# Kernel tuning notes

Measured on AMD Instinct MI355X. Metric: run time of the kernel, lower is better.

## Reference

```python
import jax, jax.numpy as jnp
import numpy as np

N = 100000
E = 1600000
IN_C, HID_C, OUT_C, NUM_CLASSES = 128, 64, 64, 40


def glorot(key, shape):
    lim = float(np.sqrt(6.0 / (shape[0] + shape[1])))
    return jax.random.uniform(key, shape, jnp.float32, -lim, lim)


def setup_inputs() -> dict:
    key = jax.random.key(0)
    ks = jax.random.split(key, 8)
    x = jax.random.normal(ks[0], (N, IN_C), jnp.float32)
    edge_index = jax.random.randint(ks[1], (2, E), 0, N, jnp.int64)
    return {
        "x": x,
        "edge_index": edge_index,
        "W1": glorot(ks[2], (IN_C, HID_C)),
        "b1": jnp.zeros((HID_C,), jnp.float32),
        "W2": glorot(ks[3], (HID_C, OUT_C)),
        "b2": jnp.zeros((OUT_C,), jnp.float32),
        "Wf": glorot(ks[4], (OUT_C, NUM_CLASSES)),
        "bf": jnp.zeros((NUM_CLASSES,), jnp.float32),
    }


def gcn_conv(x, W, b, src, dst, n):
    # PyG GCNConv: out = D^{-1/2} (A + I) D^{-1/2} (x W) + b, self-loops added.
    h = x @ W  # [N, C_out]
    loop = jnp.arange(n, dtype=src.dtype)
    src_f = jnp.concatenate([src, loop])  # [E+N]
    dst_f = jnp.concatenate([dst, loop])
    deg = jax.ops.segment_sum(jnp.ones_like(dst_f, dtype=h.dtype), dst_f,
                              num_segments=n)  # in-degree incl. self-loop
    inv_sqrt = jnp.where(deg > 0, jax.lax.rsqrt(deg), 0.0)
    norm = inv_sqrt[src_f] * inv_sqrt[dst_f]  # [E+N]
    msg = h[src_f] * norm[:, None]  # gather + scale, [E+N, C_out]
    out = jax.ops.segment_sum(msg, dst_f, num_segments=n)  # scatter-add
    return out + b


def reference(x, edge_index, W1, b1, W2, b2, Wf, bf):
    src, dst = edge_index[0], edge_index[1]
    n = x.shape[0]
    h = jax.nn.relu(gcn_conv(x, W1, b1, src, dst, n))
    h = jax.nn.relu(gcn_conv(h, W2, b2, src, dst, n))
    return h @ Wf + bf
```

## Files before the change

### kernel.cpp

```cpp
#include <hip/hip_runtime.h>

constexpr int N_NODES = 100000;
constexpr int N_EDGES = 1600000;
constexpr int IN_C  = 128;
constexpr int HID_C = 64;
constexpr int NUM_CLASSES = 40;

constexpr int BSH = 9;
constexpr int BUCK_N = 1 << BSH;
constexpr int NBUCK = (N_NODES + BUCK_N - 1) >> BSH;
constexpr int BCAP = 9216;
constexpr int FS_EPT = 16;
constexpr int FS_T = 256;
constexpr int FS_CHUNK = FS_EPT * FS_T;
constexpr int FS_BLKS = (N_EDGES + FS_CHUNK - 1) / FS_CHUNK;

typedef __attribute__((ext_vector_type(8))) short bf16x8;
typedef __attribute__((ext_vector_type(4))) short short4v;
typedef __attribute__((ext_vector_type(4))) float f32x4;

__device__ __forceinline__ unsigned short f2bf(float f) {
    unsigned u = __float_as_uint(f);
    return (unsigned short)((u + 0x7FFFu + ((u >> 16) & 1u)) >> 16);
}
__device__ __forceinline__ float bf2f(unsigned short h) {
    return __uint_as_float((unsigned)h << 16);
}

__global__ void bucket_init_kernel(unsigned* __restrict__ gcur) {
    if (threadIdx.x < NBUCK) gcur[threadIdx.x] = 0u;
}

__global__ __launch_bounds__(FS_T) void fill_stage_kernel(
        const int* __restrict__ src, const int* __restrict__ dst,
        unsigned* __restrict__ gcur, unsigned* __restrict__ stage) {
    __shared__ unsigned hist[NBUCK];
    __shared__ unsigned rbase[NBUCK];
    int t = threadIdx.x;
    for (int i = t; i < NBUCK; i += FS_T) hist[i] = 0u;
    __syncthreads();
    int e0 = blockIdx.x * FS_CHUNK + t;
    unsigned pay[FS_EPT];
    unsigned br[FS_EPT];
#pragma unroll
    for (int i = 0; i < FS_EPT; ++i) {
        int e = e0 + i * FS_T;
        br[i] = 0xFFFFFFFFu; pay[i] = 0u;
        if (e < N_EDGES) {
            unsigned d = (unsigned)dst[e];
            unsigned s = (unsigned)src[e];
            unsigned b = d >> BSH;
            unsigned r = atomicAdd(&hist[b], 1u);
            pay[i] = (s << BSH) | (d & (BUCK_N - 1u));
            br[i]  = (b << 16) | r;
        }
    }
    __syncthreads();
    for (int i = t; i < NBUCK; i += FS_T) {
        unsigned c = hist[i];
        rbase[i] = c ? ((unsigned)i * BCAP + atomicAdd(&gcur[i], c)) : 0u;
    }
    __syncthreads();
#pragma unroll
    for (int i = 0; i < FS_EPT; ++i) {
        if (br[i] != 0xFFFFFFFFu) {
            unsigned bb = br[i] >> 16;
            unsigned idx = rbase[bb] + (br[i] & 0xFFFFu);
            if (idx < (bb + 1u) * BCAP) stage[idx] = pay[i];
        }
    }
}

__global__ __launch_bounds__(256) void scan_buckets_kernel(
        const unsigned* __restrict__ gcur, unsigned* __restrict__ bbase,
        unsigned* __restrict__ rowptr) {
    __shared__ unsigned s[256];
    int t = threadIdx.x;
    unsigned v = (t < NBUCK) ? gcur[t] : 0u;
    s[t] = v;
    __syncthreads();
    for (int off = 1; off < 256; off <<= 1) {
        unsigned u = (t >= off) ? s[t - off] : 0u;
        __syncthreads();
        s[t] += u;
        __syncthreads();
    }
    if (t < NBUCK) bbase[t] = s[t] - v;
    if (t == 255) rowptr[N_NODES] = s[255];
}

__global__ __launch_bounds__(512) void fill_final_kernel(
        const unsigned* __restrict__ gcur, const unsigned* __restrict__ bbase,
        const unsigned* __restrict__ stage, unsigned* __restrict__ rowptr,
        float* __restrict__ inv, unsigned* __restrict__ csr_src) {
    __shared__ unsigned cur[BUCK_N];
    __shared__ unsigned ps[512];
    __shared__ unsigned buf[BCAP];
    int b = blockIdx.x, t = threadIdx.x;
    int lo = b << BSH;
    int nn = min(BUCK_N, N_NODES - lo);
    unsigned c = min(gcur[b], (unsigned)BCAP);
    unsigned base = bbase[b];
    const unsigned* st = stage + (size_t)b * BCAP;
    cur[t] = 0u;
    __syncthreads();
    for (int i = t; i < (int)c; i += 512) atomicAdd(&cur[st[i] & (BUCK_N - 1u)], 1u);
    __syncthreads();
    unsigned d = cur[t];
    ps[t] = d;
    __syncthreads();
    for (int off = 1; off < 512; off <<= 1) {
        unsigned u = (t >= off) ? ps[t - off] : 0u;
        __syncthreads();
        ps[t] += u;
        __syncthreads();
    }
    unsigned off0 = ps[t] - d;
    if (t < nn) {
        rowptr[lo + t] = base + off0;
        inv[lo + t] = rsqrtf((float)(d + 1u));
    }
    __syncthreads();
    cur[t] = off0;
    __syncthreads();
    for (int i = t; i < (int)c; i += 512) {
        unsigned v = st[i];
        unsigned pos = atomicAdd(&cur[v & (BUCK_N - 1u)], 1u);
        buf[pos] = v >> BSH;
    }
    __syncthreads();
    for (int i = t; i < (int)c; i += 512) csr_src[base + i] = buf[i];
}

template <int K, bool BF>
__global__ __launch_bounds__(256) void gemm_mfma_kernel(
        const void* __restrict__ Xv, const float* __restrict__ W,
        const float* __restrict__ inv, unsigned short* __restrict__ out, int n) {
    __shared__ __align__(16) short Asd[64][K + 8];
    __shared__ __align__(16) short Bsd[64][K + 8];
    int t = threadIdx.x;
    int n0 = blockIdx.x * 64;
    if (BF) {
        const uint4* Xb = (const uint4*)Xv;
        for (int i = t; i < 64 * (K / 8); i += 256) {
            int row = i / (K / 8), seg = i % (K / 8);
            int node = n0 + row;
            uint4 v = {0, 0, 0, 0};
            if (node < n) v = Xb[(size_t)node * (K / 8) + seg];
            *(uint4*)&Asd[row][seg * 8] = v;
        }
    } else {
        const float* Xf = (const float*)Xv;
        for (int i = t; i < 64 * (K / 4); i += 256) {
            int row = i / (K / 4), seg = i % (K / 4);
            int node = n0 + row;
            float4 v = {0, 0, 0, 0};
            if (node < n) v = *(const float4*)&Xf[(size_t)node * K + seg * 4];
            short4v o;
            o.x = (short)f2bf(v.x); o.y = (short)f2bf(v.y);
            o.z = (short)f2bf(v.z); o.w = (short)f2bf(v.w);
            *(short4v*)&Asd[row][seg * 4] = o;
        }
    }
    for (int i = t; i < K * 16; i += 256) {
        int k = i >> 4, ng = i & 15;
        float4 v = *(const float4*)&W[(size_t)k * 64 + ng * 4];
        Bsd[ng * 4 + 0][k] = (short)f2bf(v.x);
        Bsd[ng * 4 + 1][k] = (short)f2bf(v.y);
        Bsd[ng * 4 + 2][k] = (short)f2bf(v.z);
        Bsd[ng * 4 + 3][k] = (short)f2bf(v.w);
    }
    __syncthreads();
    int wv = t >> 6, lane = t & 63;
    int m = lane & 15, quad = lane >> 4;
    int rowbase = wv * 16;
    f32x4 acc0 = {0,0,0,0}, acc1 = {0,0,0,0}, acc2 = {0,0,0,0}, acc3 = {0,0,0,0};
#pragma unroll
    for (int kb = 0; kb < K / 32; ++kb) {
        bf16x8 af = *(const bf16x8*)&Asd[rowbase + m][kb * 32 + quad * 8];
        bf16x8 b0 = *(const bf16x8*)&Bsd[ 0 + m][kb * 32 + quad * 8];
        bf16x8 b1 = *(const bf16x8*)&Bsd[16 + m][kb * 32 + quad * 8];
        bf16x8 b2 = *(const bf16x8*)&Bsd[32 + m][kb * 32 + quad * 8];
        bf16x8 b3 = *(const bf16x8*)&Bsd[48 + m][kb * 32 + quad * 8];
        acc0 = __builtin_amdgcn_mfma_f32_16x16x32_bf16(af, b0, acc0, 0, 0, 0);
        acc1 = __builtin_amdgcn_mfma_f32_16x16x32_bf16(af, b1, acc1, 0, 0, 0);
        acc2 = __builtin_amdgcn_mfma_f32_16x16x32_bf16(af, b2, acc2, 0, 0, 0);
        acc3 = __builtin_amdgcn_mfma_f32_16x16x32_bf16(af, b3, acc3, 0, 0, 0);
    }
    f32x4 accs[4] = {acc0, acc1, acc2, acc3};
#pragma unroll
    for (int r = 0; r < 4; ++r) {
        int node = n0 + rowbase + quad * 4 + r;
        if (node < n) {
            float sc = inv[node];
#pragma unroll
            for (int s = 0; s < 4; ++s)
                out[(size_t)node * 64 + s * 16 + m] = f2bf(accs[s][r] * sc);
        }
    }
}

__global__ __launch_bounds__(256) void agg_fused_kernel(
        const unsigned* __restrict__ rowptr, const unsigned* __restrict__ csr_src,
        const unsigned short* __restrict__ hs, const float* __restrict__ inv,
        const float* __restrict__ bias, unsigned short* __restrict__ out) {
    int t = threadIdx.x;
    int lane = t & 63;
    int oct = lane >> 3;
    int cl  = lane & 7;
    int node = blockIdx.x * 32 + (t >> 6) * 8 + oct;
    unsigned beg = rowptr[node], end = rowptr[node + 1];
    float a0 = 0.f, a1 = 0.f, a2 = 0.f, a3 = 0.f;
    float a4 = 0.f, a5 = 0.f, a6 = 0.f, a7 = 0.f;
    const uint4* hsrow = (const uint4*)hs;
#pragma unroll 4
    for (unsigned e = beg; e < end; ++e) {
        unsigned s = csr_src[e];
        uint4 v = hsrow[(size_t)s * 8 + cl];
        a0 += __uint_as_float(v.x << 16);
        a1 += __uint_as_float(v.x & 0xFFFF0000u);
        a2 += __uint_as_float(v.y << 16);
        a3 += __uint_as_float(v.y & 0xFFFF0000u);
        a4 += __uint_as_float(v.z << 16);
        a5 += __uint_as_float(v.z & 0xFFFF0000u);
        a6 += __uint_as_float(v.w << 16);
        a7 += __uint_as_float(v.w & 0xFFFF0000u);
    }
    uint4 sv = hsrow[(size_t)node * 8 + cl];
    float4 bv0 = *(const float4*)&bias[cl * 8];
    float4 bv1 = *(const float4*)&bias[cl * 8 + 4];
    float s = inv[node];
    float r0 = fmaxf(s * (a0 + __uint_as_float(sv.x << 16))         + bv0.x, 0.f);
    float r1 = fmaxf(s * (a1 + __uint_as_float(sv.x & 0xFFFF0000u)) + bv0.y, 0.f);
    float r2 = fmaxf(s * (a2 + __uint_as_float(sv.y << 16))         + bv0.z, 0.f);
    float r3 = fmaxf(s * (a3 + __uint_as_float(sv.y & 0xFFFF0000u)) + bv0.w, 0.f);
    float r4 = fmaxf(s * (a4 + __uint_as_float(sv.z << 16))         + bv1.x, 0.f);
    float r5 = fmaxf(s * (a5 + __uint_as_float(sv.z & 0xFFFF0000u)) + bv1.y, 0.f);
    float r6 = fmaxf(s * (a6 + __uint_as_float(sv.w << 16))         + bv1.z, 0.f);
    float r7 = fmaxf(s * (a7 + __uint_as_float(sv.w & 0xFFFF0000u)) + bv1.w, 0.f);
    uint4 o;
    o.x = (unsigned)f2bf(r0) | ((unsigned)f2bf(r1) << 16);
    o.y = (unsigned)f2bf(r2) | ((unsigned)f2bf(r3) << 16);
    o.z = (unsigned)f2bf(r4) | ((unsigned)f2bf(r5) << 16);
    o.w = (unsigned)f2bf(r6) | ((unsigned)f2bf(r7) << 16);
    ((uint4*)out)[(size_t)node * 8 + cl] = o;
}

__global__ __launch_bounds__(320) void final_gemm_kernel(
        const unsigned short* __restrict__ H, const float* __restrict__ Wf,
        const float* __restrict__ bfv, float* __restrict__ out, int n) {
    constexpr int CK = 64, J = 40;
    __shared__ float Ws[CK * J];
    __shared__ float Hs[CK][132];
    int t = threadIdx.x;
    int n0 = blockIdx.x * 128;
    for (int i = t; i < CK * J / 4; i += 320)
        ((float4*)Ws)[i] = ((const float4*)Wf)[i];
    for (int i = t; i < 128 * 16; i += 320) {
        int row = i >> 4, kc = i & 15;
        int node = n0 + row;
        ushort4 v = {0, 0, 0, 0};
        if (node < n) v = *(const ushort4*)&H[(size_t)node * 64 + kc * 4];
        Hs[kc * 4 + 0][row] = bf2f(v.x);
        Hs[kc * 4 + 1][row] = bf2f(v.y);
        Hs[kc * 4 + 2][row] = bf2f(v.z);
        Hs[kc * 4 + 3][row] = bf2f(v.w);
    }
    __syncthreads();
    int cg = t % 10;
    int rg = t / 10;
    float4 a0 = {0,0,0,0}, a1 = {0,0,0,0}, a2 = {0,0,0,0}, a3 = {0,0,0,0};
#pragma unroll 8
    for (int k = 0; k < CK; ++k) {
        float4 b = *(const float4*)&Ws[k * J + cg * 4];
        float4 a = *(const float4*)&Hs[k][rg * 4];
        a0.x += a.x * b.x; a0.y += a.x * b.y; a0.z += a.x * b.z; a0.w += a.x * b.w;
        a1.x += a.y * b.x; a1.y += a.y * b.y; a1.z += a.y * b.z; a1.w += a.y * b.w;
        a2.x += a.z * b.x; a2.y += a.z * b.y; a2.z += a.z * b.z; a2.w += a.z * b.w;
        a3.x += a.w * b.x; a3.y += a.w * b.y; a3.z += a.w * b.z; a3.w += a.w * b.w;
    }
    float4 bv = *(const float4*)&bfv[cg * 4];
    float4 accs[4] = {a0, a1, a2, a3};
#pragma unroll
    for (int i = 0; i < 4; ++i) {
        int node = n0 + rg * 4 + i;
        if (node < n) {
            float4 r = accs[i];
            r.x += bv.x; r.y += bv.y; r.z += bv.z; r.w += bv.w;
            *(float4*)&out[(size_t)node * J + cg * 4] = r;
        }
    }
}

extern "C" void kernel_launch(void* const* d_in, const int* in_sizes, int n_in,
                              void* d_out, int out_size, void* d_ws, size_t ws_size,
                              hipStream_t stream) {
    const float* x  = (const float*)d_in[0];
    const int*   ei = (const int*)d_in[1];
    const float* W1 = (const float*)d_in[2];
    const float* b1 = (const float*)d_in[3];
    const float* W2 = (const float*)d_in[4];
    const float* b2 = (const float*)d_in[5];
    const float* Wf = (const float*)d_in[6];
    const float* bf = (const float*)d_in[7];
    float* out = (float*)d_out;

    const int* src = ei;
    const int* dst = ei + N_EDGES;

    char* ws = (char*)d_ws;
    unsigned* rowptr  = (unsigned*)(ws + 0);
    float*    inv     = (float*)   (ws + 400064);
    unsigned* gcur    = (unsigned*)(ws + 800064);
    unsigned* bbase   = (unsigned*)(ws + 800896);
    unsigned* csr_src = (unsigned*)(ws + 801792);
    unsigned short* A = (unsigned short*)(ws + 7201792);
    unsigned short* B = (unsigned short*)(ws + 20001792);
    unsigned* stage   = (unsigned*)A;

    bucket_init_kernel<<<1, 256, 0, stream>>>(gcur);
    fill_stage_kernel<<<FS_BLKS, FS_T, 0, stream>>>(src, dst, gcur, stage);
    scan_buckets_kernel<<<1, 256, 0, stream>>>(gcur, bbase, rowptr);
    fill_final_kernel<<<NBUCK, 512, 0, stream>>>(gcur, bbase, stage, rowptr, inv, csr_src);

    gemm_mfma_kernel<IN_C, false>
        <<<(N_NODES + 63) / 64, 256, 0, stream>>>(x, W1, inv, A, N_NODES);
    agg_fused_kernel<<<N_NODES / 32, 256, 0, stream>>>(rowptr, csr_src, A, inv, b1, B);

    gemm_mfma_kernel<HID_C, true>
        <<<(N_NODES + 63) / 64, 256, 0, stream>>>(B, W2, inv, A, N_NODES);
    agg_fused_kernel<<<N_NODES / 32, 256, 0, stream>>>(rowptr, csr_src, A, inv, b2, B);

    final_gemm_kernel<<<(N_NODES + 127) / 128, 320, 0, stream>>>(B, Wf, bf, out, N_NODES);
}
```

Measured before the change: 244.6 us.

## Sort nodes by degree within buckets and fold bucket scan into fill kernel

Each bucket block now runs the global bucket prefix scan itself, which removes the separate single-block scan kernel and its launch. The block also builds a per-bucket permutation of nodes sorted by in-degree, capped at 63. The aggregation kernels visit nodes through this permutation, so the 8 nodes sharing a wavefront have similar edge counts and less lane divergence and loop imbalance. The cost is a redundant small scan in every block and an extra indirection load per node, which may also scatter the output writes.

```diff
diff --git a/kernel.cpp b/kernel.cpp
--- a/kernel.cpp
+++ b/kernel.cpp
@@ -71,36 +71,31 @@
     }
 }
 
-__global__ __launch_bounds__(256) void scan_buckets_kernel(
-        const unsigned* __restrict__ gcur, unsigned* __restrict__ bbase,
-        unsigned* __restrict__ rowptr) {
-    __shared__ unsigned s[256];
-    int t = threadIdx.x;
-    unsigned v = (t < NBUCK) ? gcur[t] : 0u;
-    s[t] = v;
-    __syncthreads();
-    for (int off = 1; off < 256; off <<= 1) {
-        unsigned u = (t >= off) ? s[t - off] : 0u;
-        __syncthreads();
-        s[t] += u;
-        __syncthreads();
-    }
-    if (t < NBUCK) bbase[t] = s[t] - v;
-    if (t == 255) rowptr[N_NODES] = s[255];
-}
-
 __global__ __launch_bounds__(512) void fill_final_kernel(
-        const unsigned* __restrict__ gcur, const unsigned* __restrict__ bbase,
+        const unsigned* __restrict__ gcur,
         const unsigned* __restrict__ stage, unsigned* __restrict__ rowptr,
-        float* __restrict__ inv, unsigned* __restrict__ csr_src) {
+        float* __restrict__ inv, unsigned* __restrict__ csr_src,
+        unsigned* __restrict__ perm) {
     __shared__ unsigned cur[BUCK_N];
     __shared__ unsigned ps[512];
     __shared__ unsigned buf[BCAP];
+    __shared__ unsigned dh[64];
+    __shared__ unsigned dps[64];
     int b = blockIdx.x, t = threadIdx.x;
     int lo = b << BSH;
     int nn = min(BUCK_N, N_NODES - lo);
+    unsigned gv = (t < NBUCK) ? gcur[t] : 0u;
+    ps[t] = gv;
+    __syncthreads();
+    for (int off = 1; off < 256; off <<= 1) {
+        unsigned u = (t >= off) ? ps[t - off] : 0u;
+        __syncthreads();
+        ps[t] += u;
+        __syncthreads();
+    }
+    unsigned base = ps[b] - gcur[b];
+    if (b == NBUCK - 1 && t == 0) rowptr[N_NODES] = ps[NBUCK - 1];
     unsigned c = min(gcur[b], (unsigned)BCAP);
-    unsigned base = bbase[b];
     const unsigned* st = stage + (size_t)b * BCAP;
     cur[t] = 0u;
     __syncthreads();
@@ -120,9 +115,27 @@
         rowptr[lo + t] = base + off0;
         inv[lo + t] = rsqrtf((float)(d + 1u));
     }
-    __syncthreads();
+    if (t < 64) dh[t] = 0u;
     cur[t] = off0;
     __syncthreads();
+    unsigned key = min(d, 63u);
+    if (t < nn) atomicAdd(&dh[key], 1u);
+    __syncthreads();
+    if (t < 64) {
+        unsigned v = dh[t], sum = v;
+#pragma unroll
+        for (int off = 1; off < 64; off <<= 1) {
+            unsigned u = __shfl_up(sum, off);
+            if (t >= off) sum += u;
+        }
+        dps[t] = sum - v;
+        dh[t] = 0u;
+    }
+    __syncthreads();
+    if (t < nn) {
+        unsigned pos = dps[key] + atomicAdd(&dh[key], 1u);
+        perm[lo + pos] = (unsigned)(lo + t);
+    }
     for (int i = t; i < (int)c; i += 512) {
         unsigned v = st[i];
         unsigned pos = atomicAdd(&cur[v & (BUCK_N - 1u)], 1u);
@@ -202,13 +215,15 @@
 
 __global__ __launch_bounds__(256) void agg_fused_kernel(
         const unsigned* __restrict__ rowptr, const unsigned* __restrict__ csr_src,
+        const unsigned* __restrict__ perm,
         const unsigned short* __restrict__ hs, const float* __restrict__ inv,
         const float* __restrict__ bias, unsigned short* __restrict__ out) {
     int t = threadIdx.x;
     int lane = t & 63;
     int oct = lane >> 3;
     int cl  = lane & 7;
-    int node = blockIdx.x * 32 + (t >> 6) * 8 + oct;
+    int gid = blockIdx.x * 32 + (t >> 6) * 8 + oct;
+    int node = (int)perm[gid];
     unsigned beg = rowptr[node], end = rowptr[node + 1];
     float a0 = 0.f, a1 = 0.f, a2 = 0.f, a3 = 0.f;
     float a4 = 0.f, a5 = 0.f, a6 = 0.f, a7 = 0.f;
@@ -312,24 +327,23 @@
     unsigned* rowptr  = (unsigned*)(ws + 0);
     float*    inv     = (float*)   (ws + 400064);
     unsigned* gcur    = (unsigned*)(ws + 800064);
-    unsigned* bbase   = (unsigned*)(ws + 800896);
     unsigned* csr_src = (unsigned*)(ws + 801792);
     unsigned short* A = (unsigned short*)(ws + 7201792);
     unsigned short* B = (unsigned short*)(ws + 20001792);
+    unsigned* perm    = (unsigned*)(ws + 32801792);
     unsigned* stage   = (unsigned*)A;
 
     bucket_init_kernel<<<1, 256, 0, stream>>>(gcur);
     fill_stage_kernel<<<FS_BLKS, FS_T, 0, stream>>>(src, dst, gcur, stage);
-    scan_buckets_kernel<<<1, 256, 0, stream>>>(gcur, bbase, rowptr);
-    fill_final_kernel<<<NBUCK, 512, 0, stream>>>(gcur, bbase, stage, rowptr, inv, csr_src);
+    fill_final_kernel<<<NBUCK, 512, 0, stream>>>(gcur, stage, rowptr, inv, csr_src, perm);
 
     gemm_mfma_kernel<IN_C, false>
         <<<(N_NODES + 63) / 64, 256, 0, stream>>>(x, W1, inv, A, N_NODES);
-    agg_fused_kernel<<<N_NODES / 32, 256, 0, stream>>>(rowptr, csr_src, A, inv, b1, B);
+    agg_fused_kernel<<<N_NODES / 32, 256, 0, stream>>>(rowptr, csr_src, perm, A, inv, b1, B);
 
     gemm_mfma_kernel<HID_C, true>
         <<<(N_NODES + 63) / 64, 256, 0, stream>>>(B, W2, inv, A, N_NODES);
-    agg_fused_kernel<<<N_NODES / 32, 256, 0, stream>>>(rowptr, csr_src, A, inv, b2, B);
+    agg_fused_kernel<<<N_NODES / 32, 256, 0, stream>>>(rowptr, csr_src, perm, A, inv, b2, B);
 
     final_gemm_kernel<<<(N_NODES + 127) / 128, 320, 0, stream>>>(B, Wf, bf, out, N_NODES);
 }
```

After: 257.7 us. +5.4%, slower.
